# Kernel tuning notes

Measured on AMD Instinct MI355X. Metric: run time of the kernel, lower is better.

Reference implementation:

```python
import jax, jax.numpy as jnp
import numpy as np

G = 512        # graphs in batch
N_PER = 256    # nodes per graph (equal-size graphs)
D = 128        # embed_dim
E_PER = 4096   # edges per graph
KEEP = 0.5
K = int(np.ceil(KEEP * N_PER))  # 128 nodes kept per graph (PyG topk: ceil(ratio*n))
N = G * N_PER
E = G * E_PER


def setup_inputs() -> dict:
    key = jax.random.key(0)
    k1, k2, k3, k4, k5 = jax.random.split(key, 5)
    x = jax.random.normal(k1, (N, D), jnp.float32)
    offs = (jnp.arange(G, dtype=jnp.int32) * N_PER)[:, None]
    src = jax.random.randint(k2, (G, E_PER), 0, N_PER, dtype=jnp.int32) + offs
    dst = jax.random.randint(k3, (G, E_PER), 0, N_PER, dtype=jnp.int32) + offs
    edge_index = jnp.stack([src.reshape(-1), dst.reshape(-1)], axis=0)  # [2, E], within-graph edges
    graph_indicator = jnp.repeat(jnp.arange(G, dtype=jnp.int32), N_PER)  # [N]
    gcn_w = jax.random.normal(k4, (D, 1), jnp.float32) / np.sqrt(D)
    gcn_b = jnp.zeros((1,), jnp.float32)
    lin_w = jax.random.normal(k5, (2 * D, D), jnp.float32) / np.sqrt(2 * D)
    lin_b = jnp.zeros((D,), jnp.float32)
    return {"input_feature": x, "graph_indicator": graph_indicator, "edge_index": edge_index,
            "gcn_w": gcn_w, "gcn_b": gcn_b, "lin_w": lin_w, "lin_b": lin_b}


def gcn_conv(x, edge_index, w, b):
    # PyG GCNConv: add self-loops, symmetric normalization, aggregate at target (edge_index[1]).
    n = x.shape[0]
    loop = jnp.arange(n, dtype=edge_index.dtype)
    row = jnp.concatenate([edge_index[0], loop])  # source
    col = jnp.concatenate([edge_index[1], loop])  # target
    deg = jax.ops.segment_sum(jnp.ones_like(col, dtype=x.dtype), col, num_segments=n)
    dinv = jax.lax.rsqrt(deg)  # deg >= 1 due to self-loops
    norm = dinv[row] * dinv[col]            # [E+N]
    xw = x @ w                              # [N, out]
    msg = xw[row] * norm[:, None]           # gather + scale
    agg = jax.ops.segment_sum(msg, col, num_segments=n)
    return agg + b


def reference(input_feature, graph_indicator, edge_index, gcn_w, gcn_b, lin_w, lin_b):
    # SAGPool: attention scores via GCNConv(d -> 1)
    score = gcn_conv(input_feature, edge_index, gcn_w, gcn_b).squeeze(-1)  # [N]
    # per-graph top-k mask (equal-size graphs -> reshape)
    s = score.reshape(G, N_PER)
    _, idx = jax.lax.top_k(s, K)                                          # [G, K]
    mask = jnp.zeros((G, N_PER), bool).at[jnp.arange(G)[:, None], idx].set(True)
    # gated features of kept nodes: x[mask] * tanh(score[mask])
    feat = (input_feature * jnp.tanh(score)[:, None]).reshape(G, N_PER, D)
    m = mask[..., None]
    # global mean/max pool over kept nodes per graph (exactly K kept per graph)
    mean = jnp.sum(jnp.where(m, feat, 0.0), axis=1) / K                   # [G, D]
    mx = jnp.max(jnp.where(m, feat, -jnp.inf), axis=1)                    # [G, D]
    readout = jnp.concatenate([mean, mx], axis=1)                         # [G, 2D]
    return readout @ lin_w + lin_b                                        # [G, D]
```

## Files before the change

kernel.cpp:

```cpp
#include <hip/hip_runtime.h>
#include <math.h>

#define NG   512
#define NPER 256
#define DD   128
#define EPER 4096
#define KK   128
#define NT   1024
#define NW   16

__global__ __launch_bounds__(NT, 8) void sag_fused(
    const float* __restrict__ x,
    const int*   __restrict__ esrc,
    const int*   __restrict__ edst,
    const float* __restrict__ gcn_w,
    const float* __restrict__ gcn_b,
    const float* __restrict__ lin_w,
    const float* __restrict__ lin_b,
    float* __restrict__ out)
{
  const int g    = blockIdx.x;
  const int tid  = threadIdx.x;
  const int lane = tid & 63;
  const int wave = tid >> 6;
  const int j    = lane & 15;
  const int sub  = lane >> 4;
  const int slot = wave * 4 + sub;

  __shared__ int    sDeg[NPER];
  __shared__ int    sRank[NPER];
  __shared__ float  sXWn[NPER];
  __shared__ float  sDinv[NPER];
  __shared__ float4 sScore4[NPER / 4];
  __shared__ float2 sGF[NPER];
  __shared__ float  sPoolS[NW][DD];
  __shared__ float  sPoolM[NW][DD];
  __shared__ float2 sR2[DD];
  float* sScore = (float*)sScore4;
  float* sR     = (float*)sR2;

  const int4* es4 = (const int4*)(esrc + (size_t)g * EPER);
  const int4* ed4 = (const int4*)(edst + (size_t)g * EPER);
  int4 sa = es4[tid];
  int4 da = ed4[tid];

  const float4* xg4 = (const float4*)(x + (size_t)g * NPER * DD);
  const int colbase = slot * 32 + j;
  float4 q0[4], q1[4];
  #pragma unroll
  for (int r = 0; r < 4; ++r) {
    q0[r] = xg4[r * 2048 + colbase];
    q1[r] = xg4[r * 2048 + colbase + 16];
  }
  float4 wa = ((const float4*)gcn_w)[j];
  float4 wb = ((const float4*)gcn_w)[16 + j];

  if (tid < NPER) { sDeg[tid] = 1; sRank[tid] = 0; }
  __syncthreads();

  atomicAdd(&sDeg[da.x & 255], 1);
  atomicAdd(&sDeg[da.y & 255], 1);
  atomicAdd(&sDeg[da.z & 255], 1);
  atomicAdd(&sDeg[da.w & 255], 1);

  #pragma unroll
  for (int r = 0; r < 4; ++r) {
    float acc = q0[r].x*wa.x + q0[r].y*wa.y + q0[r].z*wa.z + q0[r].w*wa.w
              + q1[r].x*wb.x + q1[r].y*wb.y + q1[r].z*wb.z + q1[r].w*wb.w;
    acc += __shfl_xor(acc, 1);
    acc += __shfl_xor(acc, 2);
    acc += __shfl_xor(acc, 4);
    acc += __shfl_xor(acc, 8);
    if (j == 0) sXWn[r * 64 + slot] = acc;
  }
  __syncthreads();

  if (tid < NPER) {
    float dv = 1.0f / sqrtf((float)sDeg[tid]);
    float xw = sXWn[tid];
    sDinv[tid]  = dv;
    sXWn[tid]   = xw * dv;
    sScore[tid] = xw * dv * dv;
  }
  __syncthreads();

  {
    int s0 = sa.x & 255, d0 = da.x & 255;
    int s1 = sa.y & 255, d1 = da.y & 255;
    int s2 = sa.z & 255, d2 = da.z & 255;
    int s3 = sa.w & 255, d3 = da.w & 255;
    atomicAdd(&sScore[d0], sXWn[s0] * sDinv[d0]);
    atomicAdd(&sScore[d1], sXWn[s1] * sDinv[d1]);
    atomicAdd(&sScore[d2], sXWn[s2] * sDinv[d2]);
    atomicAdd(&sScore[d3], sXWn[s3] * sDinv[d3]);
  }
  __syncthreads();

  {
    int node = tid & 255;
    int seg  = tid >> 8;
    float s_i = sScore[node];
    int base = seg * 16;
    int part = 0;
    #pragma unroll 8
    for (int t = 0; t < 16; ++t) {
      float4 v = sScore4[base + t];
      int jj = (base + t) * 4;
      part += (v.x > s_i) || (v.x == s_i && (jj + 0) < node);
      part += (v.y > s_i) || (v.y == s_i && (jj + 1) < node);
      part += (v.z > s_i) || (v.z == s_i && (jj + 2) < node);
      part += (v.w > s_i) || (v.w == s_i && (jj + 3) < node);
    }
    atomicAdd(&sRank[node], part);
  }
  __syncthreads();

  if (tid < NPER) {
    bool kp = sRank[tid] < KK;
    float gate = tanhf(sScore[tid] + gcn_b[0]);
    sGF[tid] = make_float2(kp ? gate : 0.0f, kp ? 0.0f : INFINITY);
  }
  __syncthreads();

  float su0=0,su1=0,su2=0,su3=0,su4=0,su5=0,su6=0,su7=0;
  float mx0=-INFINITY,mx1=-INFINITY,mx2=-INFINITY,mx3=-INFINITY;
  float mx4=-INFINITY,mx5=-INFINITY,mx6=-INFINITY,mx7=-INFINITY;
  #pragma unroll
  for (int r = 0; r < 4; ++r) {
    float2 gf = sGF[r * 64 + slot];
    float g1 = gf.x, fb = gf.y;
    float a;
    a = q0[r].x * g1; su0 += a; mx0 = fmaxf(mx0, a - fb);
    a = q0[r].y * g1; su1 += a; mx1 = fmaxf(mx1, a - fb);
    a = q0[r].z * g1; su2 += a; mx2 = fmaxf(mx2, a - fb);
    a = q0[r].w * g1; su3 += a; mx3 = fmaxf(mx3, a - fb);
    a = q1[r].x * g1; su4 += a; mx4 = fmaxf(mx4, a - fb);
    a = q1[r].y * g1; su5 += a; mx5 = fmaxf(mx5, a - fb);
    a = q1[r].z * g1; su6 += a; mx6 = fmaxf(mx6, a - fb);
    a = q1[r].w * g1; su7 += a; mx7 = fmaxf(mx7, a - fb);
  }
  #define RED_S(v) v += __shfl_xor(v,16); v += __shfl_xor(v,32);
  #define RED_M(v) v = fmaxf(v,__shfl_xor(v,16)); v = fmaxf(v,__shfl_xor(v,32));
  RED_S(su0) RED_S(su1) RED_S(su2) RED_S(su3)
  RED_S(su4) RED_S(su5) RED_S(su6) RED_S(su7)
  RED_M(mx0) RED_M(mx1) RED_M(mx2) RED_M(mx3)
  RED_M(mx4) RED_M(mx5) RED_M(mx6) RED_M(mx7)
  if (sub == 0) {
    ((float4*)&sPoolS[wave][4 * j])[0]      = make_float4(su0, su1, su2, su3);
    ((float4*)&sPoolS[wave][64 + 4 * j])[0] = make_float4(su4, su5, su6, su7);
    ((float4*)&sPoolM[wave][4 * j])[0]      = make_float4(mx0, mx1, mx2, mx3);
    ((float4*)&sPoolM[wave][64 + 4 * j])[0] = make_float4(mx4, mx5, mx6, mx7);
  }
  __syncthreads();

  if (tid < DD) {
    float s = 0.f;
    #pragma unroll
    for (int w = 0; w < NW; ++w) s += sPoolS[w][tid];
    sR[tid] = s * (1.0f / KK);
  } else if (tid < 2 * DD) {
    int d = tid - DD;
    float m = -INFINITY;
    #pragma unroll
    for (int w = 0; w < NW; ++w) m = fmaxf(m, sPoolM[w][d]);
    sR[tid] = m;
  }
  __syncthreads();

  const float2* lw2 = (const float2*)lin_w;
  float a0 = 0.f, a1 = 0.f;
  #pragma unroll
  for (int t = 0; t < 8; ++t) {
    int k2 = wave * 8 + t;
    float2 rv = sR2[k2];
    float2 p0 = lw2[(2 * k2) * 64 + lane];
    float2 p1 = lw2[(2 * k2 + 1) * 64 + lane];
    a0 += rv.x * p0.x + rv.y * p1.x;
    a1 += rv.x * p0.y + rv.y * p1.y;
  }
  float2* sP2 = (float2*)sPoolS;
  sP2[wave * 64 + lane] = make_float2(a0, a1);
  __syncthreads();
  if (wave == 0) {
    float2 a = sP2[lane];
    #pragma unroll
    for (int w = 1; w < NW; ++w) { float2 p = sP2[w * 64 + lane]; a.x += p.x; a.y += p.y; }
    float2 bb = ((const float2*)lin_b)[lane];
    a.x += bb.x; a.y += bb.y;
    ((float2*)out)[(size_t)g * 64 + lane] = a;
  }
}

extern "C" void kernel_launch(void* const* d_in, const int* in_sizes, int n_in,
                              void* d_out, int out_size, void* d_ws, size_t ws_size,
                              hipStream_t stream) {
  const float* x  = (const float*)d_in[0];
  const int*   ei = (const int*)d_in[2];
  const float* gw = (const float*)d_in[3];
  const float* gb = (const float*)d_in[4];
  const float* lw = (const float*)d_in[5];
  const float* lb = (const float*)d_in[6];
  float* out = (float*)d_out;
  const int E = in_sizes[2] / 2;
  sag_fused<<<NG, NT, 0, stream>>>(x, ei, ei + E, gw, gb, lw, lb, out);
}
```

Baseline: 128.2 us.

## Stage per-graph feature tile in dynamic LDS instead of holding it in registers

Each thread now writes its loaded x rows into a 128KB dynamic shared-memory buffer and re-reads them for the gated mean/max pooling, rather than keeping them live in registers across the whole kernel. All static shared arrays move into one dynamic buffer, the launch-bounds hint drops from 8 to 4, and the host raises the dynamic LDS limit once. The aim is to relieve register pressure, but the roughly 152KB LDS footprint allows only one 1024-thread block per CU. That halves or worse the concurrent blocks available to hide memory latency.

```diff
diff --git a/kernel.cpp b/kernel.cpp
--- a/kernel.cpp
+++ b/kernel.cpp
@@ -9,7 +9,9 @@
 #define NT   1024
 #define NW   16
 
-__global__ __launch_bounds__(NT, 8) void sag_fused(
+#define SMEM_BYTES 155648
+
+__global__ __launch_bounds__(NT, 4) void sag_fused(
     const float* __restrict__ x,
     const int*   __restrict__ esrc,
     const int*   __restrict__ edst,
@@ -27,17 +29,19 @@
   const int sub  = lane >> 4;
   const int slot = wave * 4 + sub;
 
-  __shared__ int    sDeg[NPER];
-  __shared__ int    sRank[NPER];
-  __shared__ float  sXWn[NPER];
-  __shared__ float  sDinv[NPER];
-  __shared__ float4 sScore4[NPER / 4];
-  __shared__ float2 sGF[NPER];
-  __shared__ float  sPoolS[NW][DD];
-  __shared__ float  sPoolM[NW][DD];
-  __shared__ float2 sR2[DD];
-  float* sScore = (float*)sScore4;
-  float* sR     = (float*)sR2;
+  extern __shared__ __align__(16) char smem[];
+  float4* sX4     = (float4*)(smem);
+  float4* sScore4 = (float4*)(smem + 131072);
+  float2* sGF     = (float2*)(smem + 132096);
+  float*  sPoolS  = (float*)(smem + 134144);
+  float*  sPoolM  = (float*)(smem + 142336);
+  float2* sR2     = (float2*)(smem + 150528);
+  int*    sDeg    = (int*)(smem + 151552);
+  int*    sRank   = (int*)(smem + 152576);
+  float*  sXWn    = (float*)(smem + 153600);
+  float*  sDinv   = (float*)(smem + 154624);
+  float*  sScore  = (float*)sScore4;
+  float*  sR      = (float*)sR2;
 
   const int4* es4 = (const int4*)(esrc + (size_t)g * EPER);
   const int4* ed4 = (const int4*)(edst + (size_t)g * EPER);
@@ -65,6 +69,8 @@
 
   #pragma unroll
   for (int r = 0; r < 4; ++r) {
+    sX4[r * 2048 + colbase]      = q0[r];
+    sX4[r * 2048 + colbase + 16] = q1[r];
     float acc = q0[r].x*wa.x + q0[r].y*wa.y + q0[r].z*wa.z + q0[r].w*wa.w
               + q1[r].x*wb.x + q1[r].y*wb.y + q1[r].z*wb.z + q1[r].w*wb.w;
     acc += __shfl_xor(acc, 1);
@@ -128,16 +134,18 @@
   #pragma unroll
   for (int r = 0; r < 4; ++r) {
     float2 gf = sGF[r * 64 + slot];
+    float4 v0 = sX4[r * 2048 + colbase];
+    float4 v1 = sX4[r * 2048 + colbase + 16];
     float g1 = gf.x, fb = gf.y;
     float a;
-    a = q0[r].x * g1; su0 += a; mx0 = fmaxf(mx0, a - fb);
-    a = q0[r].y * g1; su1 += a; mx1 = fmaxf(mx1, a - fb);
-    a = q0[r].z * g1; su2 += a; mx2 = fmaxf(mx2, a - fb);
-    a = q0[r].w * g1; su3 += a; mx3 = fmaxf(mx3, a - fb);
-    a = q1[r].x * g1; su4 += a; mx4 = fmaxf(mx4, a - fb);
-    a = q1[r].y * g1; su5 += a; mx5 = fmaxf(mx5, a - fb);
-    a = q1[r].z * g1; su6 += a; mx6 = fmaxf(mx6, a - fb);
-    a = q1[r].w * g1; su7 += a; mx7 = fmaxf(mx7, a - fb);
+    a = v0.x * g1; su0 += a; mx0 = fmaxf(mx0, a - fb);
+    a = v0.y * g1; su1 += a; mx1 = fmaxf(mx1, a - fb);
+    a = v0.z * g1; su2 += a; mx2 = fmaxf(mx2, a - fb);
+    a = v0.w * g1; su3 += a; mx3 = fmaxf(mx3, a - fb);
+    a = v1.x * g1; su4 += a; mx4 = fmaxf(mx4, a - fb);
+    a = v1.y * g1; su5 += a; mx5 = fmaxf(mx5, a - fb);
+    a = v1.z * g1; su6 += a; mx6 = fmaxf(mx6, a - fb);
+    a = v1.w * g1; su7 += a; mx7 = fmaxf(mx7, a - fb);
   }
   #define RED_S(v) v += __shfl_xor(v,16); v += __shfl_xor(v,32);
   #define RED_M(v) v = fmaxf(v,__shfl_xor(v,16)); v = fmaxf(v,__shfl_xor(v,32));
@@ -146,23 +154,23 @@
   RED_M(mx0) RED_M(mx1) RED_M(mx2) RED_M(mx3)
   RED_M(mx4) RED_M(mx5) RED_M(mx6) RED_M(mx7)
   if (sub == 0) {
-    ((float4*)&sPoolS[wave][4 * j])[0]      = make_float4(su0, su1, su2, su3);
-    ((float4*)&sPoolS[wave][64 + 4 * j])[0] = make_float4(su4, su5, su6, su7);
-    ((float4*)&sPoolM[wave][4 * j])[0]      = make_float4(mx0, mx1, mx2, mx3);
-    ((float4*)&sPoolM[wave][64 + 4 * j])[0] = make_float4(mx4, mx5, mx6, mx7);
+    ((float4*)&sPoolS[wave * DD + 4 * j])[0]      = make_float4(su0, su1, su2, su3);
+    ((float4*)&sPoolS[wave * DD + 64 + 4 * j])[0] = make_float4(su4, su5, su6, su7);
+    ((float4*)&sPoolM[wave * DD + 4 * j])[0]      = make_float4(mx0, mx1, mx2, mx3);
+    ((float4*)&sPoolM[wave * DD + 64 + 4 * j])[0] = make_float4(mx4, mx5, mx6, mx7);
   }
   __syncthreads();
 
   if (tid < DD) {
     float s = 0.f;
     #pragma unroll
-    for (int w = 0; w < NW; ++w) s += sPoolS[w][tid];
+    for (int w = 0; w < NW; ++w) s += sPoolS[w * DD + tid];
     sR[tid] = s * (1.0f / KK);
   } else if (tid < 2 * DD) {
     int d = tid - DD;
     float m = -INFINITY;
     #pragma unroll
-    for (int w = 0; w < NW; ++w) m = fmaxf(m, sPoolM[w][d]);
+    for (int w = 0; w < NW; ++w) m = fmaxf(m, sPoolM[w * DD + d]);
     sR[tid] = m;
   }
   __syncthreads();
@@ -194,6 +202,12 @@
 extern "C" void kernel_launch(void* const* d_in, const int* in_sizes, int n_in,
                               void* d_out, int out_size, void* d_ws, size_t ws_size,
                               hipStream_t stream) {
+  static bool s_init = false;
+  if (!s_init) {
+    (void)hipFuncSetAttribute((const void*)sag_fused,
+                              hipFuncAttributeMaxDynamicSharedMemorySize, SMEM_BYTES);
+    s_init = true;
+  }
   const float* x  = (const float*)d_in[0];
   const int*   ei = (const int*)d_in[2];
   const float* gw = (const float*)d_in[3];
@@ -202,5 +216,5 @@
   const float* lb = (const float*)d_in[6];
   float* out = (float*)d_out;
   const int E = in_sizes[2] / 2;
-  sag_fused<<<NG, NT, 0, stream>>>(x, ei, ei + E, gw, gb, lw, lb, out);
+  sag_fused<<<NG, NT, SMEM_BYTES, stream>>>(x, ei, ei + E, gw, gb, lw, lb, out);
 }
```

Result: slower. 137.7 us (+7.4%).
